# Kernel optimization log

Measured on AMD Instinct MI355X. Metric: run time of the kernel, lower is better.

Reference implementation:

```python
import jax, jax.numpy as jnp
import numpy as np

B, S, D = 4, 4096, 2048

def setup_inputs() -> dict:
    key = jax.random.key(0)
    k1, k2 = jax.random.split(key)
    k = jax.random.normal(k1, (B, S, D), dtype=jnp.float32)
    v = jax.random.normal(k2, (B, S, D), dtype=jnp.float32)
    kv_state = jnp.zeros((D, D), dtype=jnp.float32)
    k_sum = jnp.zeros((D,), dtype=jnp.float32)
    return {"k": k, "v": v, "kv_state": kv_state, "k_sum": k_sum}

def reference(k, v, kv_state, k_sum):
    b, s, d = k.shape
    k_flat = k.reshape(-1, d)  # (N, D), N = B*S
    v_flat = v.reshape(-1, d)
    # Accumulate outer-product state: kv_state += sum_i k_i v_i^T
    kv_new = kv_state + jnp.einsum('nd,ne->de', k_flat, v_flat)
    ks_new = k_sum + k_flat.sum(axis=0)
    # Readout: context = k @ kv_state^T ; normalizer = k @ k_sum
    context = jnp.einsum('nd,ed->ne', k_flat, kv_new).reshape(b, s, d)
    normalizer = (k_flat @ ks_new).reshape(b, s, 1)
    return context, normalizer
```

## Files before the change

kernel.cpp:

```cpp
#include <hip/hip_runtime.h>
#include <hip/hip_bf16.h>
#include <cstdio>
#include <cstdint>

#define NBIG 16384
#define DDIM 2048
#define SPLITK 4

#define BM 256
#define BN 256
#define BKT 64

typedef __attribute__((ext_vector_type(4))) float f32x4;
typedef __attribute__((ext_vector_type(8))) short bf16x8;

__device__ __forceinline__ unsigned short f2bf(float f) {
  union { float f; unsigned u; } v; v.f = f;
  return (unsigned short)((v.u + 0x7FFFu + ((v.u >> 16) & 1u)) >> 16);
}

__device__ __forceinline__ void gll16(const void* g, void* l) {
  auto gp = reinterpret_cast<const __attribute__((address_space(1))) unsigned int*>(
      reinterpret_cast<uintptr_t>(g));
  auto lp = reinterpret_cast<__attribute__((address_space(3))) unsigned int*>(
      (unsigned int)reinterpret_cast<uintptr_t>(l));
  __builtin_amdgcn_global_load_lds(gp, lp, 16, 0, 0);
}

__device__ __forceinline__ void waitvm8() { asm volatile("s_waitcnt vmcnt(8)" ::: "memory"); }
__device__ __forceinline__ void waitvm0() { asm volatile("s_waitcnt vmcnt(0)" ::: "memory"); }
__device__ __forceinline__ void waitlgkm0() { asm volatile("s_waitcnt lgkmcnt(0)" ::: "memory"); }
__device__ __forceinline__ void barrier_pinned() {
  __builtin_amdgcn_sched_barrier(0);
  __builtin_amdgcn_s_barrier();
  __builtin_amdgcn_sched_barrier(0);
}

__device__ __forceinline__ void xcd_swizzle(int& bx, int& by, int& bz) {
  const unsigned nx = gridDim.x, ny = gridDim.y;
  const unsigned nwg = nx * ny * gridDim.z;
  unsigned wg = blockIdx.x + nx * (blockIdx.y + ny * blockIdx.z);
  wg = (wg & 7u) * (nwg >> 3) + (wg >> 3);
  bx = wg % nx;
  unsigned r = wg / nx;
  by = r % ny;
  bz = r / ny;
}

__global__ __launch_bounds__(256) void prep_kernel(
    const float* __restrict__ k, const float* __restrict__ v,
    unsigned short* __restrict__ KT, unsigned short* __restrict__ VT,
    unsigned short* __restrict__ Kbf, float* __restrict__ ks)
{
  __shared__ unsigned short sm[64][66];
  __shared__ float sks[64];
  const int t = threadIdx.x;
  const int tiles_d = DDIM / 64;
  const int n0 = (blockIdx.x / tiles_d) * 64;
  const int d0 = (blockIdx.x % tiles_d) * 64;
  const bool is_k = (blockIdx.y == 0);
  const float* __restrict__ src = is_k ? k : v;
  unsigned short* __restrict__ dstT = is_k ? KT : VT;

  const int r = t >> 4;
  const int c = (t & 15) * 4;

  if (t < 64) sks[t] = 0.f;
  __syncthreads();

  float a0 = 0.f, a1 = 0.f, a2 = 0.f, a3 = 0.f;
#pragma unroll
  for (int i = 0; i < 4; ++i) {
    const int row = i * 16 + r;
    f32x4 val = *reinterpret_cast<const f32x4*>(&src[(size_t)(n0 + row) * DDIM + d0 + c]);
    unsigned short b0 = f2bf(val.x), b1 = f2bf(val.y), b2 = f2bf(val.z), b3 = f2bf(val.w);
    sm[row][c + 0] = b0; sm[row][c + 1] = b1;
    sm[row][c + 2] = b2; sm[row][c + 3] = b3;
    if (is_k) {
      unsigned int p0 = (unsigned)b0 | ((unsigned)b1 << 16);
      unsigned int p1 = (unsigned)b2 | ((unsigned)b3 << 16);
      *reinterpret_cast<uint2*>(&Kbf[(size_t)(n0 + row) * DDIM + d0 + c]) = make_uint2(p0, p1);
      a0 += val.x; a1 += val.y; a2 += val.z; a3 += val.w;
    }
  }
  if (is_k) {
    atomicAdd(&sks[c + 0], a0);
    atomicAdd(&sks[c + 1], a1);
    atomicAdd(&sks[c + 2], a2);
    atomicAdd(&sks[c + 3], a3);
  }
  __syncthreads();

#pragma unroll
  for (int i = 0; i < 4; ++i) {
    const int rowp = i * 16 + r;
    unsigned int p0 = (unsigned)sm[c + 0][rowp] | ((unsigned)sm[c + 1][rowp] << 16);
    unsigned int p1 = (unsigned)sm[c + 2][rowp] | ((unsigned)sm[c + 3][rowp] << 16);
    *reinterpret_cast<uint2*>(&dstT[(size_t)(d0 + rowp) * NBIG + n0 + c]) = make_uint2(p0, p1);
  }
  if (is_k && t < 64) atomicAdd(&ks[d0 + t], sks[t]);
}

__global__ void init_ks_kernel(const float* __restrict__ ksum, float* __restrict__ ks) {
  int i = blockIdx.x * 256 + threadIdx.x;
  if (i < DDIM) ks[i] = ksum[i];
}

__global__ __launch_bounds__(512, 2) void gemm256_kernel(
    const unsigned short* __restrict__ A, const unsigned short* __restrict__ B,
    float* __restrict__ C, int lda, int ldb, int kchunk, long long zstride)
{
  __shared__ unsigned short Abuf[2][BM * BKT];
  __shared__ unsigned short Bbuf[2][BN * BKT];

  int bx, by, bz;
  xcd_swizzle(bx, by, bz);

  const int t = threadIdx.x, lane = t & 63, w = t >> 6;
  const int wm = w >> 2, wn = w & 3;
  const int m0 = by * BM, n0 = bx * BN;
  const int kbeg = bz * kchunk;
  const int NT = kchunk / BKT;

  const int srow = lane >> 3;
  const int sgr  = (lane & 7) ^ srow;
  const unsigned short* Ag = A + (size_t)(m0 + srow) * lda + kbeg + sgr * 8;
  const unsigned short* Bg = B + (size_t)(n0 + srow) * ldb + kbeg + sgr * 8;

  const int hi = lane >> 4;
  const int lo7 = lane & 7;
  const int swz0 = ((0 + hi) ^ lo7) * 8;
  const int swz1 = ((4 + hi) ^ lo7) * 8;
  const int arow = (wm * 128 + (lane & 15)) * BKT;
  const int brow = (wn * 64 + (lane & 15)) * BKT;

  auto stage_op = [&](const unsigned short* G, unsigned short* Lbase, int ld_,
                      int kt, int half) {
    const unsigned short* g = G + (size_t)(half * 128 + w * 16) * ld_ + (size_t)kt * BKT;
    unsigned short* l = Lbase + (half * 128 + w * 16) * BKT;
    gll16(g, l);
    gll16(g + (size_t)8 * ld_, l + 8 * BKT);
  };

  stage_op(Bg, Bbuf[0], ldb, 0, 0); stage_op(Bg, Bbuf[0], ldb, 0, 1);
  stage_op(Ag, Abuf[0], lda, 0, 0); stage_op(Ag, Abuf[0], lda, 0, 1);
  stage_op(Bg, Bbuf[1], ldb, 1, 0); stage_op(Bg, Bbuf[1], ldb, 1, 1);
  stage_op(Ag, Abuf[1], lda, 1, 0); stage_op(Ag, Abuf[1], lda, 1, 1);
  waitvm8();
  __builtin_amdgcn_s_barrier();
  __builtin_amdgcn_sched_barrier(0);

  f32x4 acc[8][4] = {};

#pragma unroll 2
  for (int tl = 0; tl < NT; ++tl) {
    const int q = tl & 1;
    const unsigned short* Al = Abuf[q];
    const unsigned short* Bl = Bbuf[q];
    const bool pf = (tl + 2 < NT);
    bf16x8 af[8][2], bb[4][2];

#pragma unroll
    for (int m = 0; m < 8; ++m) {
      af[m][0] = *reinterpret_cast<const bf16x8*>(Al + arow + m * 16 * BKT + swz0);
      af[m][1] = *reinterpret_cast<const bf16x8*>(Al + arow + m * 16 * BKT + swz1);
    }
#pragma unroll
    for (int n = 0; n < 4; ++n) {
      bb[n][0] = *reinterpret_cast<const bf16x8*>(Bl + brow + n * 16 * BKT + swz0);
      bb[n][1] = *reinterpret_cast<const bf16x8*>(Bl + brow + n * 16 * BKT + swz1);
    }

    __builtin_amdgcn_s_setprio(1);
#pragma unroll
    for (int kk = 0; kk < 2; ++kk)
#pragma unroll
      for (int m = 0; m < 4; ++m)
#pragma unroll
        for (int n = 0; n < 4; ++n)
          acc[m][n] = __builtin_amdgcn_mfma_f32_16x16x32_bf16(af[m][kk], bb[n][kk], acc[m][n], 0, 0, 0);
    __builtin_amdgcn_s_setprio(0);

    waitlgkm0();
    barrier_pinned();

    if (pf) {
      stage_op(Bg, Bbuf[q], ldb, tl + 2, 0);
      stage_op(Bg, Bbuf[q], ldb, tl + 2, 1);
      stage_op(Ag, Abuf[q], lda, tl + 2, 0);
      stage_op(Ag, Abuf[q], lda, tl + 2, 1);
    }

    __builtin_amdgcn_s_setprio(1);
#pragma unroll
    for (int kk = 0; kk < 2; ++kk)
#pragma unroll
      for (int m = 4; m < 8; ++m)
#pragma unroll
        for (int n = 0; n < 4; ++n)
          acc[m][n] = __builtin_amdgcn_mfma_f32_16x16x32_bf16(af[m][kk], bb[n][kk], acc[m][n], 0, 0, 0);
    __builtin_amdgcn_s_setprio(0);
    __builtin_amdgcn_sched_barrier(0);

    if (tl + 1 < NT) {
      if (pf) waitvm8();
      else    waitvm0();
      __builtin_amdgcn_s_barrier();
      __builtin_amdgcn_sched_barrier(0);
    }
  }

  float* Cz = C + (size_t)bz * zstride;
  const int crow0 = m0 + wm * 128 + hi * 4;
  const int ccol0 = n0 + wn * 64 + (lane & 15);
#pragma unroll
  for (int m = 0; m < 8; ++m)
#pragma unroll
    for (int n = 0; n < 4; ++n)
#pragma unroll
      for (int j = 0; j < 4; ++j)
        Cz[(size_t)(crow0 + m * 16 + j) * DDIM + ccol0 + n * 16] = acc[m][n][j];
}

__global__ __launch_bounds__(256) void kvconv_kernel(
    const float* __restrict__ kvp, const float* __restrict__ kvst,
    unsigned short* __restrict__ kvbf)
{
  size_t i = ((size_t)blockIdx.x * 256 + threadIdx.x) * 4;
  f32x4 s = *reinterpret_cast<const f32x4*>(&kvst[i]);
#pragma unroll
  for (int z = 0; z < SPLITK; ++z) {
    f32x4 p = *reinterpret_cast<const f32x4*>(&kvp[(size_t)z * DDIM * DDIM + i]);
    s.x += p.x; s.y += p.y; s.z += p.z; s.w += p.w;
  }
  unsigned int p0 = (unsigned)f2bf(s.x) | ((unsigned)f2bf(s.y) << 16);
  unsigned int p1 = (unsigned)f2bf(s.z) | ((unsigned)f2bf(s.w) << 16);
  *reinterpret_cast<uint2*>(&kvbf[i]) = make_uint2(p0, p1);
}

__global__ __launch_bounds__(256) void norm_kernel(
    const unsigned short* __restrict__ Kbf, const float* __restrict__ ks,
    float* __restrict__ out)
{
  const int lane = threadIdx.x & 63;
  const int w = threadIdx.x >> 6;
  const int row = blockIdx.x * 4 + w;
  const unsigned short* kr = Kbf + (size_t)row * DDIM;
  float s = 0.f;
#pragma unroll
  for (int i = 0; i < 4; ++i) {
    bf16x8 a = *reinterpret_cast<const bf16x8*>(&kr[i * 512 + lane * 8]);
    f32x4 b0 = *reinterpret_cast<const f32x4*>(&ks[i * 512 + lane * 8]);
    f32x4 b1 = *reinterpret_cast<const f32x4*>(&ks[i * 512 + lane * 8 + 4]);
    float af[8];
#pragma unroll
    for (int j = 0; j < 8; ++j) {
      union { unsigned u; float f; } cv;
      cv.u = ((unsigned)(unsigned short)a[j]) << 16;
      af[j] = cv.f;
    }
    s += af[0] * b0.x + af[1] * b0.y + af[2] * b0.z + af[3] * b0.w
       + af[4] * b1.x + af[5] * b1.y + af[6] * b1.z + af[7] * b1.w;
  }
  for (int off = 32; off; off >>= 1) s += __shfl_down(s, off, 64);
  if (lane == 0) out[row] = s;
}

extern "C" void kernel_launch(void* const* d_in, const int* in_sizes, int n_in,
                              void* d_out, int out_size, void* d_ws, size_t ws_size,
                              hipStream_t stream) {
  const float* k    = (const float*)d_in[0];
  const float* v    = (const float*)d_in[1];
  const float* kvst = (const float*)d_in[2];
  const float* ksum = (const float*)d_in[3];

  const size_t SZ_T = (size_t)DDIM * NBIG * 2;
  const size_t WS_NEED = SZ_T * 3 + (size_t)DDIM * DDIM * 2 + DDIM * 4;
  if (ws_size < WS_NEED) {
    fprintf(stderr, "kernel_launch: ws too small %zu < %zu\n", ws_size, WS_NEED);
    return;
  }
  char* ws = (char*)d_ws;
  unsigned short* KT   = (unsigned short*)ws;
  unsigned short* VT   = (unsigned short*)(ws + SZ_T);
  unsigned short* Kbf  = (unsigned short*)(ws + 2 * SZ_T);
  unsigned short* KVbf = (unsigned short*)(ws + 3 * SZ_T);
  float* ks            = (float*)(ws + 3 * SZ_T + (size_t)DDIM * DDIM * 2);

  float* ctx = (float*)d_out;
  float* nrm = ctx + (size_t)NBIG * DDIM;
  float* kvp = ctx;

  init_ks_kernel<<<(DDIM + 255) / 256, 256, 0, stream>>>(ksum, ks);
  prep_kernel<<<dim3((NBIG / 64) * (DDIM / 64), 2), 256, 0, stream>>>(k, v, KT, VT, Kbf, ks);
  gemm256_kernel<<<dim3(DDIM / BN, DDIM / BM, SPLITK), 512, 0, stream>>>(
      KT, VT, kvp, NBIG, NBIG, NBIG / SPLITK, (long long)DDIM * DDIM);
  kvconv_kernel<<<(DDIM * DDIM) / (256 * 4), 256, 0, stream>>>(kvp, kvst, KVbf);
  gemm256_kernel<<<dim3(DDIM / BN, NBIG / BM, 1), 512, 0, stream>>>(
      Kbf, KVbf, ctx, DDIM, DDIM, DDIM, 0);
  norm_kernel<<<NBIG / 4, 256, 0, stream>>>(Kbf, ks, nrm);
}
```

Measured before the change: 386.1 us.

## Switch GEMM to 4 waves with 128x128 per-wave tiles, drop split MFMA phases

```diff
diff --git a/kernel.cpp b/kernel.cpp
--- a/kernel.cpp
+++ b/kernel.cpp
@@ -27,14 +27,10 @@
   __builtin_amdgcn_global_load_lds(gp, lp, 16, 0, 0);
 }
 
-__device__ __forceinline__ void waitvm8() { asm volatile("s_waitcnt vmcnt(8)" ::: "memory"); }
-__device__ __forceinline__ void waitvm0() { asm volatile("s_waitcnt vmcnt(0)" ::: "memory"); }
+__device__ __forceinline__ void waitvm16() { asm volatile("s_waitcnt vmcnt(16)" ::: "memory"); }
+__device__ __forceinline__ void waitvm0()  { asm volatile("s_waitcnt vmcnt(0)" ::: "memory"); }
 __device__ __forceinline__ void waitlgkm0() { asm volatile("s_waitcnt lgkmcnt(0)" ::: "memory"); }
-__device__ __forceinline__ void barrier_pinned() {
-  __builtin_amdgcn_sched_barrier(0);
-  __builtin_amdgcn_s_barrier();
-  __builtin_amdgcn_sched_barrier(0);
-}
+#define SB0 __builtin_amdgcn_sched_barrier(0)
 
 __device__ __forceinline__ void xcd_swizzle(int& bx, int& by, int& bz) {
   const unsigned nx = gridDim.x, ny = gridDim.y;
@@ -106,7 +102,7 @@
   if (i < DDIM) ks[i] = ksum[i];
 }
 
-__global__ __launch_bounds__(512, 2) void gemm256_kernel(
+__global__ __launch_bounds__(256, 1) void gemm256_kernel(
     const unsigned short* __restrict__ A, const unsigned short* __restrict__ B,
     float* __restrict__ C, int lda, int ldb, int kchunk, long long zstride)
 {
@@ -116,49 +112,50 @@
   int bx, by, bz;
   xcd_swizzle(bx, by, bz);
 
-  const int t = threadIdx.x, lane = t & 63, w = t >> 6;
-  const int wm = w >> 2, wn = w & 3;
+  const int t = threadIdx.x, lane = t & 63, wv = t >> 6;
+  const int wm = wv >> 1, wn = wv & 1;
   const int m0 = by * BM, n0 = bx * BN;
   const int kbeg = bz * kchunk;
   const int NT = kchunk / BKT;
-
-  const int srow = lane >> 3;
-  const int sgr  = (lane & 7) ^ srow;
-  const unsigned short* Ag = A + (size_t)(m0 + srow) * lda + kbeg + sgr * 8;
-  const unsigned short* Bg = B + (size_t)(n0 + srow) * ldb + kbeg + sgr * 8;
+  const int wvbase = wv * 64;
 
   const int hi = lane >> 4;
   const int lo7 = lane & 7;
   const int swz0 = ((0 + hi) ^ lo7) * 8;
   const int swz1 = ((4 + hi) ^ lo7) * 8;
   const int arow = (wm * 128 + (lane & 15)) * BKT;
-  const int brow = (wn * 64 + (lane & 15)) * BKT;
-
-  auto stage_op = [&](const unsigned short* G, unsigned short* Lbase, int ld_,
-                      int kt, int half) {
-    const unsigned short* g = G + (size_t)(half * 128 + w * 16) * ld_ + (size_t)kt * BKT;
-    unsigned short* l = Lbase + (half * 128 + w * 16) * BKT;
-    gll16(g, l);
-    gll16(g + (size_t)8 * ld_, l + 8 * BKT);
+  const int brow = (wn * 128 + (lane & 15)) * BKT;
+
+  auto stage_tile = [&](const unsigned short* G, int ld_, unsigned short* Lbase, int kt) {
+#pragma unroll
+    for (int i = 0; i < 8; ++i) {
+      const int g = i * 256 + t;
+      const int row = g >> 3;
+      const int gc = (g & 7) ^ (row & 7);
+      const unsigned short* src = G + (size_t)row * ld_ + (size_t)kt * BKT + gc * 8;
+      gll16(src, Lbase + (size_t)(i * 256 + wvbase) * 8);
+    }
   };
 
-  stage_op(Bg, Bbuf[0], ldb, 0, 0); stage_op(Bg, Bbuf[0], ldb, 0, 1);
-  stage_op(Ag, Abuf[0], lda, 0, 0); stage_op(Ag, Abuf[0], lda, 0, 1);
-  stage_op(Bg, Bbuf[1], ldb, 1, 0); stage_op(Bg, Bbuf[1], ldb, 1, 1);
-  stage_op(Ag, Abuf[1], lda, 1, 0); stage_op(Ag, Abuf[1], lda, 1, 1);
-  waitvm8();
+  const unsigned short* Ag = A + (size_t)m0 * lda + kbeg;
+  const unsigned short* Bg = B + (size_t)n0 * ldb + kbeg;
+
+  stage_tile(Bg, ldb, Bbuf[0], 0);
+  stage_tile(Ag, lda, Abuf[0], 0);
+  stage_tile(Bg, ldb, Bbuf[1], 1);
+  stage_tile(Ag, lda, Abuf[1], 1);
+  waitvm16();
   __builtin_amdgcn_s_barrier();
-  __builtin_amdgcn_sched_barrier(0);
-
-  f32x4 acc[8][4] = {};
-
-#pragma unroll 2
+  SB0;
+
+  f32x4 acc[8][8] = {};
+
   for (int tl = 0; tl < NT; ++tl) {
     const int q = tl & 1;
     const unsigned short* Al = Abuf[q];
     const unsigned short* Bl = Bbuf[q];
     const bool pf = (tl + 2 < NT);
-    bf16x8 af[8][2], bb[4][2];
+    bf16x8 af[8][2], bf[8][2];
 
 #pragma unroll
     for (int m = 0; m < 8; ++m) {
@@ -166,57 +163,41 @@
       af[m][1] = *reinterpret_cast<const bf16x8*>(Al + arow + m * 16 * BKT + swz1);
     }
 #pragma unroll
-    for (int n = 0; n < 4; ++n) {
-      bb[n][0] = *reinterpret_cast<const bf16x8*>(Bl + brow + n * 16 * BKT + swz0);
-      bb[n][1] = *reinterpret_cast<const bf16x8*>(Bl + brow + n * 16 * BKT + swz1);
-    }
-
-    __builtin_amdgcn_s_setprio(1);
+    for (int n = 0; n < 8; ++n) {
+      bf[n][0] = *reinterpret_cast<const bf16x8*>(Bl + brow + n * 16 * BKT + swz0);
+      bf[n][1] = *reinterpret_cast<const bf16x8*>(Bl + brow + n * 16 * BKT + swz1);
+    }
+
 #pragma unroll
     for (int kk = 0; kk < 2; ++kk)
 #pragma unroll
-      for (int m = 0; m < 4; ++m)
-#pragma unroll
-        for (int n = 0; n < 4; ++n)
-          acc[m][n] = __builtin_amdgcn_mfma_f32_16x16x32_bf16(af[m][kk], bb[n][kk], acc[m][n], 0, 0, 0);
-    __builtin_amdgcn_s_setprio(0);
+      for (int m = 0; m < 8; ++m)
+#pragma unroll
+        for (int n = 0; n < 8; ++n)
+          acc[m][n] = __builtin_amdgcn_mfma_f32_16x16x32_bf16(af[m][kk], bf[n][kk], acc[m][n], 0, 0, 0);
 
     waitlgkm0();
-    barrier_pinned();
+    SB0; __builtin_amdgcn_s_barrier(); SB0;
 
     if (pf) {
-      stage_op(Bg, Bbuf[q], ldb, tl + 2, 0);
-      stage_op(Bg, Bbuf[q], ldb, tl + 2, 1);
-      stage_op(Ag, Abuf[q], lda, tl + 2, 0);
-      stage_op(Ag, Abuf[q], lda, tl + 2, 1);
-    }
-
-    __builtin_amdgcn_s_setprio(1);
-#pragma unroll
-    for (int kk = 0; kk < 2; ++kk)
-#pragma unroll
-      for (int m = 4; m < 8; ++m)
-#pragma unroll
-        for (int n = 0; n < 4; ++n)
-          acc[m][n] = __builtin_amdgcn_mfma_f32_16x16x32_bf16(af[m][kk], bb[n][kk], acc[m][n], 0, 0, 0);
-    __builtin_amdgcn_s_setprio(0);
-    __builtin_amdgcn_sched_barrier(0);
-
+      stage_tile(Bg, ldb, Bbuf[q], tl + 2);
+      stage_tile(Ag, lda, Abuf[q], tl + 2);
+    }
     if (tl + 1 < NT) {
-      if (pf) waitvm8();
+      if (pf) waitvm16();
       else    waitvm0();
       __builtin_amdgcn_s_barrier();
-      __builtin_amdgcn_sched_barrier(0);
+      SB0;
     }
   }
 
   float* Cz = C + (size_t)bz * zstride;
   const int crow0 = m0 + wm * 128 + hi * 4;
-  const int ccol0 = n0 + wn * 64 + (lane & 15);
+  const int ccol0 = n0 + wn * 128 + (lane & 15);
 #pragma unroll
   for (int m = 0; m < 8; ++m)
 #pragma unroll
-    for (int n = 0; n < 4; ++n)
+    for (int n = 0; n < 8; ++n)
 #pragma unroll
       for (int j = 0; j < 4; ++j)
         Cz[(size_t)(crow0 + m * 16 + j) * DDIM + ccol0 + n * 16] = acc[m][n][j];
@@ -293,10 +274,10 @@
 
   init_ks_kernel<<<(DDIM + 255) / 256, 256, 0, stream>>>(ksum, ks);
   prep_kernel<<<dim3((NBIG / 64) * (DDIM / 64), 2), 256, 0, stream>>>(k, v, KT, VT, Kbf, ks);
-  gemm256_kernel<<<dim3(DDIM / BN, DDIM / BM, SPLITK), 512, 0, stream>>>(
+  gemm256_kernel<<<dim3(DDIM / BN, DDIM / BM, SPLITK), 256, 0, stream>>>(
       KT, VT, kvp, NBIG, NBIG, NBIG / SPLITK, (long long)DDIM * DDIM);
   kvconv_kernel<<<(DDIM * DDIM) / (256 * 4), 256, 0, stream>>>(kvp, kvst, KVbf);
-  gemm256_kernel<<<dim3(DDIM / BN, NBIG / BM, 1), 512, 0, stream>>>(
+  gemm256_kernel<<<dim3(DDIM / BN, NBIG / BM, 1), 256, 0, stream>>>(
       Kbf, KVbf, ctx, DDIM, DDIM, DDIM, 0);
   norm_kernel<<<NBIG / 4, 256, 0, stream>>>(Kbf, ks, nrm);
 }
```

New measurement: 431.2 us. +11.7%, slower.
